# Kernel tuning notes

Measured on AMD Instinct MI355X. Metric: run time of the kernel, lower is better.

## Reference

```python
import jax, jax.numpy as jnp
import numpy as np
import math

_PI = math.pi

@jax.custom_vjp
def atan_spike(h):
    # Heaviside forward, ATan surrogate (alpha=2.0) backward
    return (h >= 0).astype(h.dtype)

def _atan_fwd(h):
    return (h >= 0).astype(h.dtype), h

def _atan_bwd(h, g):
    # d/dh [ (1/pi) atan(pi*h) + 1/2 ] = 1 / (1 + (pi*h)^2)
    return (g / (1.0 + (_PI * h) ** 2),)

atan_spike.defvjp(_atan_fwd, _atan_bwd)

def plif_scan(x, alpha, v_th):
    # x: [T, ...]; PLIF: v += alpha*(x - v); spike; hard reset to 0
    a = alpha.reshape(())
    def step(v, xt):
        v = v + a * (xt - v)
        s = atan_spike(v - v_th)
        v = v * (1.0 - s)
        return v, s
    v0 = jnp.zeros_like(x[0])
    _, spikes = jax.lax.scan(step, v0, x)
    return spikes

def setup_inputs() -> dict:
    key = jax.random.key(0)
    k1, k2, k3 = jax.random.split(key, 3)
    T, B, N, D, H = 4, 8, 1024, 512, 2048
    x = jax.random.normal(k1, (T, B, N, D), dtype=jnp.float32)
    W1 = jax.random.normal(k2, (H, D), dtype=jnp.float32) * (1.0 / math.sqrt(D))
    W2 = jax.random.normal(k3, (D, H), dtype=jnp.float32) * (1.0 / math.sqrt(H))
    alpha1 = jnp.full((1,), 0.5, dtype=jnp.float32)  # 1/tau, tau=2.0
    alpha2 = jnp.full((1,), 0.5, dtype=jnp.float32)
    return {"x": x, "W1": W1, "W2": W2, "alpha1": alpha1, "alpha2": alpha2}

def reference(x, W1, W2, alpha1, alpha2):
    V_TH = 1.0
    h = jnp.einsum('tbnd,hd->tbnh', x, W1)      # fc1 (no bias)
    s1 = plif_scan(h, alpha1, V_TH)             # PLIF neuron 1
    y = jnp.einsum('tbnh,dh->tbnd', s1, W2)     # fc2 (no bias)
    s2 = plif_scan(y, alpha2, V_TH)             # PLIF neuron 2
    return s2
```

## Files before the change

### kernel.cpp

```cpp
#include <hip/hip_runtime.h>

#define T_  4
#define BN_ 8192
#define D_  512
#define H_  2048

typedef float f4 __attribute__((ext_vector_type(4)));
typedef float f32x4 __attribute__((ext_vector_type(4)));
typedef _Float16 f16x8 __attribute__((ext_vector_type(8)));

__device__ __forceinline__ void split8(const f4 u0, const f4 u1, f16x8& hi, f16x8& lo) {
#pragma unroll
    for (int i = 0; i < 4; ++i) {
        _Float16 a = (_Float16)u0[i]; hi[i]     = a; lo[i]     = (_Float16)(u0[i] - (float)a);
        _Float16 b = (_Float16)u1[i]; hi[4 + i] = b; lo[4 + i] = (_Float16)(u1[i] - (float)b);
    }
}

__device__ __forceinline__ void spikes4_to_f16(unsigned b, unsigned& lo, unsigned& hi) {
    const unsigned p0 = (b & 0xFFu) | ((b & 0xFF00u) << 8);
    const unsigned p1 = ((b >> 16) & 0xFFu) | ((b >> 8) & 0xFF0000u);
    lo = p0 * 0x3C00u;
    hi = p1 * 0x3C00u;
}

__device__ __forceinline__ void glds16(const void* g, void* l) {
    __builtin_amdgcn_global_load_lds((const __attribute__((address_space(1))) unsigned int*)g,
                                     (__attribute__((address_space(3))) unsigned int*)l, 16, 0, 0);
}

__global__ __launch_bounds__(256)
void k_split(const float* __restrict__ x, _Float16* __restrict__ xs)
{
    const int b   = blockIdx.x;
    const int t   = b & 3;
    const int k0B = (b >> 2) & 15;
    const int bnB = b >> 6;
    const int kg  = threadIdx.x & 3;
    const int row = threadIdx.x >> 2;

    const float* src = x + ((size_t)t * BN_ + bnB * 64 + row) * D_ + k0B * 32 + kg * 8;
    const f4 u0 = *(const f4*)src;
    const f4 u1 = *(const f4*)(src + 4);
    f16x8 hi, lo;
    split8(u0, u1, hi, lo);

    const size_t base = ((size_t)(bnB * 16 + k0B) * 4 + t) * 4096;
    *(f16x8*)&xs[base +        kg * 512 + row * 8] = hi;
    *(f16x8*)&xs[base + 2048 + kg * 512 + row * 8] = lo;
}

__global__ __launch_bounds__(256)
void k_splitW(const float* __restrict__ W1, _Float16* __restrict__ w1s)
{
    const int gid = blockIdx.x * 256 + threadIdx.x;
    const int col = gid & 127;
    const int kg  = (gid >> 7) & 3;
    const int kb  = (gid >> 9) & 15;
    const int h0b = gid >> 13;

    const float* src = W1 + (size_t)(h0b * 128 + col) * D_ + kb * 32 + kg * 8;
    const f4 u0 = *(const f4*)src;
    const f4 u1 = *(const f4*)(src + 4);
    f16x8 hi, lo;
    split8(u0, u1, hi, lo);

    const size_t base = (size_t)(h0b * 16 + kb) * 8192;
    *(f16x8*)&w1s[base +        kg * 1024 + col * 8] = hi;
    *(f16x8*)&w1s[base + 4096 + kg * 1024 + col * 8] = lo;
}

__global__ __launch_bounds__(256, 2)
void k_fc1b(const _Float16* __restrict__ xs, const _Float16* __restrict__ w1s,
            const float* __restrict__ alphap, unsigned char* __restrict__ s1)
{
    __shared__ _Float16 Ab[2][T_][2][4][64][8];

    const int tid  = threadIdx.x;
    const int lane = tid & 63;
    const int w    = tid >> 6;
    const int wr   = (w >> 1) * 32;
    const int wc   = (w & 1) * 64;

    const int gid   = blockIdx.x;
    const int panel = gid >> 8;
    const int h0i   = (gid >> 4) & 15;
    const int bnL   = gid & 15;
    const int bnB   = panel * 16 + bnL;
    const int bn0   = bnB * 64;
    const int h0    = h0i * 128;

    const int l15 = lane & 15;
    const int kgl = lane >> 4;
    const int lq  = kgl * 4;

    const float a1v = alphap[0];

    f32x4 acc[T_][2][4];
#pragma unroll
    for (int t = 0; t < T_; ++t)
#pragma unroll
        for (int m = 0; m < 2; ++m)
#pragma unroll
            for (int n = 0; n < 4; ++n) acc[t][m][n] = (f32x4){0.f, 0.f, 0.f, 0.f};

    const char* xbase = (const char*)xs + (size_t)bnB * 16 * 32768;
    const _Float16* bl = w1s + (size_t)h0i * (16 * 8192)
                             + (size_t)kgl * 1024 + (size_t)(wc + l15) * 8;

#define FC1_GLDS(BUF, KB)                                                        \
    {                                                                            \
        const char* cb_ = xbase + (size_t)(KB) * 32768;                          \
        _Float16* lA_ = &Ab[BUF][0][0][0][0][0];                                 \
        _Pragma("unroll")                                                        \
        for (int i_ = 0; i_ < 8; ++i_) {                                         \
            const int c_ = i_ * 4 + w;                                           \
            glds16(cb_ + c_ * 1024 + lane * 16, lA_ + c_ * 512);                 \
        }                                                                        \
    }

#define FC1_BLOAD(KB, B0, B1)                                                    \
    {                                                                            \
        const _Float16* bp_ = bl + (size_t)(KB) * 8192;                          \
        _Pragma("unroll")                                                        \
        for (int n_ = 0; n_ < 4; ++n_) {                                         \
            B0[n_] = *(const f16x8*)(bp_ + n_ * 128);                            \
            B1[n_] = *(const f16x8*)(bp_ + 4096 + n_ * 128);                     \
        }                                                                        \
    }

#define FC1_COMPUTE(BUF, B0, B1)                                                 \
    _Pragma("unroll")                                                            \
    for (int t_ = 0; t_ < T_; ++t_)                                              \
        _Pragma("unroll")                                                        \
        for (int m_ = 0; m_ < 2; ++m_) {                                         \
            const f16x8 a0_ = *(const f16x8*)&Ab[BUF][t_][0][kgl][wr + m_ * 16 + l15][0]; \
            const f16x8 a1_ = *(const f16x8*)&Ab[BUF][t_][1][kgl][wr + m_ * 16 + l15][0]; \
            _Pragma("unroll")                                                    \
            for (int n_ = 0; n_ < 4; ++n_) {                                     \
                acc[t_][m_][n_] = __builtin_amdgcn_mfma_f32_16x16x32_f16(a0_, B0[n_], acc[t_][m_][n_], 0, 0, 0); \
                acc[t_][m_][n_] = __builtin_amdgcn_mfma_f32_16x16x32_f16(a0_, B1[n_], acc[t_][m_][n_], 0, 0, 0); \
                acc[t_][m_][n_] = __builtin_amdgcn_mfma_f32_16x16x32_f16(a1_, B0[n_], acc[t_][m_][n_], 0, 0, 0); \
            }                                                                    \
        }

    f16x8 bA0[4], bA1[4], bB0[4], bB1[4];

    FC1_GLDS(0, 0)
    FC1_BLOAD(0, bA0, bA1)
    __syncthreads();

#pragma unroll 1
    for (int it = 0; it < 8; ++it) {
        const int kb = 2 * it;
        FC1_GLDS(1, kb + 1)
        FC1_BLOAD(kb + 1, bB0, bB1)
        FC1_COMPUTE(0, bA0, bA1)
        __syncthreads();
        if (it < 7) {
            FC1_GLDS(0, kb + 2)
            FC1_BLOAD(kb + 2, bA0, bA1)
        }
        FC1_COMPUTE(1, bB0, bB1)
        __syncthreads();
    }

#pragma unroll
    for (int m = 0; m < 2; ++m)
#pragma unroll
        for (int n = 0; n < 4; ++n)
#pragma unroll
            for (int q = 0; q < 4; ++q) {
                float v = 0.f;
#pragma unroll
                for (int t = 0; t < T_; ++t) {
                    v = v + a1v * (acc[t][m][n][q] - v);
                    const bool sp = (v >= 1.0f);
                    s1[((size_t)t * BN_ + bn0 + wr + m * 16 + lq + q) * H_ +
                       (h0 + wc + n * 16 + l15)] = sp ? (unsigned char)1 : (unsigned char)0;
                    if (sp) v = 0.f;
                }
            }
}

__global__ __launch_bounds__(256, 2)
void k_fc1(const _Float16* __restrict__ xs, const float* __restrict__ W1,
           const float* __restrict__ alphap, unsigned char* __restrict__ s1)
{
    __shared__ _Float16 Ab[T_][2][4][64][8];
    __shared__ _Float16 Bb[2][4][128][8];

    const int tid  = threadIdx.x;
    const int lane = tid & 63;
    const int w    = tid >> 6;
    const int wr   = (w >> 1) * 32;
    const int wc   = (w & 1) * 64;
    const int bnB  = blockIdx.x;
    const int bn0  = bnB * 64;
    const int h0   = blockIdx.y * 128;

    const int l15 = lane & 15;
    const int kgl = lane >> 4;
    const int lq  = kgl * 4;

    const int bcol = tid & 127;
    const int bkh  = tid >> 7;

    const float a1v = alphap[0];

    f32x4 acc[T_][2][4];
#pragma unroll
    for (int t = 0; t < T_; ++t)
#pragma unroll
        for (int m = 0; m < 2; ++m)
#pragma unroll
            for (int n = 0; n < 4; ++n) acc[t][m][n] = (f32x4){0.f, 0.f, 0.f, 0.f};

    const char* xbase = (const char*)xs + (size_t)bnB * 16 * 32768;
    const float* wp0  = W1 + (size_t)(h0 + bcol) * D_ + bkh * 16;

    f4 w0 = *(const f4*)wp0,       w1 = *(const f4*)(wp0 + 4);
    f4 w2 = *(const f4*)(wp0 + 8), w3 = *(const f4*)(wp0 + 12);

    for (int kb = 0; kb < 16; ++kb) {
        __syncthreads();
        const char* cb = xbase + (size_t)kb * 32768;
        _Float16* lA = &Ab[0][0][0][0][0];
#pragma unroll
        for (int i = 0; i < 8; ++i) {
            const int c = i * 4 + w;
            glds16(cb + c * 1024 + lane * 16, lA + c * 512);
        }
        {
            f16x8 hA, lA2, hB, lB;
            split8(w0, w1, hA, lA2); split8(w2, w3, hB, lB);
            *(f16x8*)&Bb[0][2 * bkh][bcol][0]     = hA;
            *(f16x8*)&Bb[0][2 * bkh + 1][bcol][0] = hB;
            *(f16x8*)&Bb[1][2 * bkh][bcol][0]     = lA2;
            *(f16x8*)&Bb[1][2 * bkh + 1][bcol][0] = lB;
        }
        if (kb < 15) {
            const float* wp = wp0 + (kb + 1) * 32;
            w0 = *(const f4*)wp;       w1 = *(const f4*)(wp + 4);
            w2 = *(const f4*)(wp + 8); w3 = *(const f4*)(wp + 12);
        }
        __syncthreads();

        f16x8 bf0[4], bf1[4];
#pragma unroll
        for (int n = 0; n < 4; ++n) {
            bf0[n] = *(const f16x8*)&Bb[0][kgl][wc + n * 16 + l15][0];
            bf1[n] = *(const f16x8*)&Bb[1][kgl][wc + n * 16 + l15][0];
        }
#pragma unroll
        for (int t = 0; t < T_; ++t)
#pragma unroll
            for (int m = 0; m < 2; ++m) {
                const f16x8 a0 = *(const f16x8*)&Ab[t][0][kgl][wr + m * 16 + l15][0];
                const f16x8 a1 = *(const f16x8*)&Ab[t][1][kgl][wr + m * 16 + l15][0];
#pragma unroll
                for (int n = 0; n < 4; ++n) {
                    acc[t][m][n] = __builtin_amdgcn_mfma_f32_16x16x32_f16(a0, bf0[n], acc[t][m][n], 0, 0, 0);
                    acc[t][m][n] = __builtin_amdgcn_mfma_f32_16x16x32_f16(a0, bf1[n], acc[t][m][n], 0, 0, 0);
                    acc[t][m][n] = __builtin_amdgcn_mfma_f32_16x16x32_f16(a1, bf0[n], acc[t][m][n], 0, 0, 0);
                }
            }
    }

#pragma unroll
    for (int m = 0; m < 2; ++m)
#pragma unroll
        for (int n = 0; n < 4; ++n)
#pragma unroll
            for (int q = 0; q < 4; ++q) {
                float v = 0.f;
#pragma unroll
                for (int t = 0; t < T_; ++t) {
                    v = v + a1v * (acc[t][m][n][q] - v);
                    const bool sp = (v >= 1.0f);
                    s1[((size_t)t * BN_ + bn0 + wr + m * 16 + lq + q) * H_ +
                       (h0 + wc + n * 16 + l15)] = sp ? (unsigned char)1 : (unsigned char)0;
                    if (sp) v = 0.f;
                }
            }
}

__global__ __launch_bounds__(256, 2)
void k_fc2(const unsigned char* __restrict__ s1, const float* __restrict__ W2,
           const float* __restrict__ alphap, float* __restrict__ out)
{
    __shared__ _Float16 A2[2][4][4][64][8];
    __shared__ _Float16 B2[2][2][4][128][8];

    const int tid  = threadIdx.x;
    const int lane = tid & 63;
    const int w    = tid >> 6;
    const int wr   = (w >> 1) * 32;
    const int wc   = (w & 1) * 64;
    const int bn0  = blockIdx.x * 64;
    const int d0   = blockIdx.y * 128;

    const int l15 = lane & 15;
    const int kgl = lane >> 4;
    const int lq  = kgl * 4;

    const int bcol = tid & 127;
    const int bkh  = tid >> 7;
    const int at   = tid >> 6;
    const int arow = lane;

    const float a2v = alphap[0];

    f32x4 acc[T_][2][4];
#pragma unroll
    for (int t = 0; t < T_; ++t)
#pragma unroll
        for (int m = 0; m < 2; ++m)
#pragma unroll
            for (int n = 0; n < 4; ++n) acc[t][m][n] = (f32x4){0.f, 0.f, 0.f, 0.f};

    const unsigned char* ap = s1 + ((size_t)at * BN_ + bn0 + arow) * H_;
    const float*         wp0 = W2 + (size_t)(d0 + bcol) * H_ + bkh * 16;

    {
        const uint4 r0 = *(const uint4*)(ap);
        const uint4 r1 = *(const uint4*)(ap + 16);
        unsigned v[8];
        spikes4_to_f16(r0.x, v[0], v[1]); spikes4_to_f16(r0.y, v[2], v[3]);
        spikes4_to_f16(r0.z, v[4], v[5]); spikes4_to_f16(r0.w, v[6], v[7]);
        *(uint4*)&A2[0][at][0][arow][0] = *(const uint4*)&v[0];
        *(uint4*)&A2[0][at][1][arow][0] = *(const uint4*)&v[4];
        spikes4_to_f16(r1.x, v[0], v[1]); spikes4_to_f16(r1.y, v[2], v[3]);
        spikes4_to_f16(r1.z, v[4], v[5]); spikes4_to_f16(r1.w, v[6], v[7]);
        *(uint4*)&A2[0][at][2][arow][0] = *(const uint4*)&v[0];
        *(uint4*)&A2[0][at][3][arow][0] = *(const uint4*)&v[4];

        const f4 w0 = *(const f4*)wp0, w1 = *(const f4*)(wp0 + 4);
        const f4 w2 = *(const f4*)(wp0 + 8), w3 = *(const f4*)(wp0 + 12);
        f16x8 hA, lA, hB, lB;
        split8(w0, w1, hA, lA); split8(w2, w3, hB, lB);
        *(f16x8*)&B2[0][0][2 * bkh][bcol][0]     = hA;
        *(f16x8*)&B2[0][0][2 * bkh + 1][bcol][0] = hB;
        *(f16x8*)&B2[0][1][2 * bkh][bcol][0]     = lA;
        *(f16x8*)&B2[0][1][2 * bkh + 1][bcol][0] = lB;
    }
    __syncthreads();

    int cur = 0;
    for (int kb = 0; kb < 64; ++kb) {
        uint4 r0, r1; f4 w0, w1, w2, w3;
        if (kb < 63) {
            r0 = *(const uint4*)(ap + (kb + 1) * 32);
            r1 = *(const uint4*)(ap + (kb + 1) * 32 + 16);
            const float* wp = wp0 + (kb + 1) * 32;
            w0 = *(const f4*)wp;       w1 = *(const f4*)(wp + 4);
            w2 = *(const f4*)(wp + 8); w3 = *(const f4*)(wp + 12);
        }

        f16x8 bf0[4], bf1[4];
#pragma unroll
        for (int n = 0; n < 4; ++n) {
            bf0[n] = *(const f16x8*)&B2[cur][0][kgl][wc + n * 16 + l15][0];
            bf1[n] = *(const f16x8*)&B2[cur][1][kgl][wc + n * 16 + l15][0];
        }
#pragma unroll
        for (int t = 0; t < T_; ++t)
#pragma unroll
            for (int m = 0; m < 2; ++m) {
                const f16x8 af = *(const f16x8*)&A2[cur][t][kgl][wr + m * 16 + l15][0];
#pragma unroll
                for (int n = 0; n < 4; ++n) {
                    acc[t][m][n] = __builtin_amdgcn_mfma_f32_16x16x32_f16(af, bf0[n], acc[t][m][n], 0, 0, 0);
                    acc[t][m][n] = __builtin_amdgcn_mfma_f32_16x16x32_f16(af, bf1[n], acc[t][m][n], 0, 0, 0);
                }
            }

        if (kb < 63) {
            unsigned v[8];
            spikes4_to_f16(r0.x, v[0], v[1]); spikes4_to_f16(r0.y, v[2], v[3]);
            spikes4_to_f16(r0.z, v[4], v[5]); spikes4_to_f16(r0.w, v[6], v[7]);
            *(uint4*)&A2[cur ^ 1][at][0][arow][0] = *(const uint4*)&v[0];
            *(uint4*)&A2[cur ^ 1][at][1][arow][0] = *(const uint4*)&v[4];
            spikes4_to_f16(r1.x, v[0], v[1]); spikes4_to_f16(r1.y, v[2], v[3]);
            spikes4_to_f16(r1.z, v[4], v[5]); spikes4_to_f16(r1.w, v[6], v[7]);
            *(uint4*)&A2[cur ^ 1][at][2][arow][0] = *(const uint4*)&v[0];
            *(uint4*)&A2[cur ^ 1][at][3][arow][0] = *(const uint4*)&v[4];

            f16x8 hA, lA, hB, lB;
            split8(w0, w1, hA, lA); split8(w2, w3, hB, lB);
            *(f16x8*)&B2[cur ^ 1][0][2 * bkh][bcol][0]     = hA;
            *(f16x8*)&B2[cur ^ 1][0][2 * bkh + 1][bcol][0] = hB;
            *(f16x8*)&B2[cur ^ 1][1][2 * bkh][bcol][0]     = lA;
            *(f16x8*)&B2[cur ^ 1][1][2 * bkh + 1][bcol][0] = lB;
        }
        __syncthreads();
        cur ^= 1;
    }

#pragma unroll
    for (int m = 0; m < 2; ++m)
#pragma unroll
        for (int n = 0; n < 4; ++n)
#pragma unroll
            for (int q = 0; q < 4; ++q) {
                float v = 0.f;
#pragma unroll
                for (int t = 0; t < T_; ++t) {
                    v = v + a2v * (acc[t][m][n][q] - v);
                    const bool sp = (v >= 1.0f);
                    out[((size_t)t * BN_ + bn0 + wr + m * 16 + lq + q) * D_ +
                        (d0 + wc + n * 16 + l15)] = sp ? 1.0f : 0.0f;
                    if (sp) v = 0.f;
                }
            }
}

extern "C" void kernel_launch(void* const* d_in, const int* in_sizes, int n_in,
                              void* d_out, int out_size, void* d_ws, size_t ws_size,
                              hipStream_t stream) {
    const float* x      = (const float*)d_in[0];
    const float* W1     = (const float*)d_in[1];
    const float* W2     = (const float*)d_in[2];
    const float* alpha1 = (const float*)d_in[3];
    const float* alpha2 = (const float*)d_in[4];
    float* out = (float*)d_out;

    unsigned char* s1 = (unsigned char*)d_ws;
    _Float16* xs = (_Float16*)d_out;
    const size_t S1_BYTES = (size_t)T_ * BN_ * H_;
    const size_t W1S_BYTES = (size_t)H_ * D_ * 2 * sizeof(_Float16);

    k_split<<<dim3(8192), dim3(256), 0, stream>>>(x, xs);

    if (ws_size >= S1_BYTES + W1S_BYTES) {
        _Float16* w1s = (_Float16*)((char*)d_ws + S1_BYTES);
        k_splitW<<<dim3(512), dim3(256), 0, stream>>>(W1, w1s);
        k_fc1b<<<dim3(2048), dim3(256), 0, stream>>>(xs, w1s, alpha1, s1);
    } else {
        k_fc1<<<dim3(128, 16), dim3(256), 0, stream>>>(xs, W1, alpha1, s1);
    }
    k_fc2<<<dim3(128, 4), dim3(256), 0, stream>>>(s1, W2, alpha2, out);
}
```

Measured before the change: 310.0 us.

## Pre-split W2 into fp16 hi/lo tiles and stream B operands from registers in fc2

Adds a k_splitW2 kernel that converts W2 once into MFMA-ready fp16 hi/lo tiles in the workspace. A new k_fc2b loads these B fragments straight into registers with prefetch, so only the spike A tile is staged in LDS with double buffering. The fc1b main loop changes from a manually two-way unrolled loop to a single loop with a buffer index and register copies. This trades an extra prep kernel and more workspace for less LDS traffic and no per-block fp32-to-fp16 splitting of W2.

```diff
diff --git a/kernel.cpp b/kernel.cpp
--- a/kernel.cpp
+++ b/kernel.cpp
@@ -68,6 +68,26 @@
     const size_t base = (size_t)(h0b * 16 + kb) * 8192;
     *(f16x8*)&w1s[base +        kg * 1024 + col * 8] = hi;
     *(f16x8*)&w1s[base + 4096 + kg * 1024 + col * 8] = lo;
+}
+
+__global__ __launch_bounds__(256)
+void k_splitW2(const float* __restrict__ W2, _Float16* __restrict__ w2s)
+{
+    const int gid = blockIdx.x * 256 + threadIdx.x;
+    const int col = gid & 127;
+    const int kg  = (gid >> 7) & 3;
+    const int kb  = (gid >> 9) & 63;
+    const int d0b = gid >> 15;
+
+    const float* src = W2 + (size_t)(d0b * 128 + col) * H_ + kb * 32 + kg * 8;
+    const f4 u0 = *(const f4*)src;
+    const f4 u1 = *(const f4*)(src + 4);
+    f16x8 hi, lo;
+    split8(u0, u1, hi, lo);
+
+    const size_t base = (size_t)(d0b * 64 + kb) * 8192;
+    *(f16x8*)&w2s[base +        kg * 1024 + col * 8] = hi;
+    *(f16x8*)&w2s[base + 4096 + kg * 1024 + col * 8] = lo;
 }
 
 __global__ __launch_bounds__(256, 2)
@@ -144,25 +164,25 @@
             }                                                                    \
         }
 
-    f16x8 bA0[4], bA1[4], bB0[4], bB1[4];
+    f16x8 bc0[4], bc1[4], bpA0[4], bpA1[4];
 
     FC1_GLDS(0, 0)
-    FC1_BLOAD(0, bA0, bA1)
+    FC1_BLOAD(0, bc0, bc1)
     __syncthreads();
 
-#pragma unroll 1
-    for (int it = 0; it < 8; ++it) {
-        const int kb = 2 * it;
-        FC1_GLDS(1, kb + 1)
-        FC1_BLOAD(kb + 1, bB0, bB1)
-        FC1_COMPUTE(0, bA0, bA1)
+    int buf = 0;
+    for (int kb = 0; kb < 16; ++kb) {
+        if (kb < 15) {
+            FC1_GLDS(buf ^ 1, kb + 1)
+            FC1_BLOAD(kb + 1, bpA0, bpA1)
+        }
+        FC1_COMPUTE(buf, bc0, bc1)
         __syncthreads();
-        if (it < 7) {
-            FC1_GLDS(0, kb + 2)
-            FC1_BLOAD(kb + 2, bA0, bA1)
-        }
-        FC1_COMPUTE(1, bB0, bB1)
-        __syncthreads();
+        if (kb < 15) {
+#pragma unroll
+            for (int n = 0; n < 4; ++n) { bc0[n] = bpA0[n]; bc1[n] = bpA1[n]; }
+        }
+        buf ^= 1;
     }
 
 #pragma unroll
@@ -280,6 +300,125 @@
                     const bool sp = (v >= 1.0f);
                     s1[((size_t)t * BN_ + bn0 + wr + m * 16 + lq + q) * H_ +
                        (h0 + wc + n * 16 + l15)] = sp ? (unsigned char)1 : (unsigned char)0;
+                    if (sp) v = 0.f;
+                }
+            }
+}
+
+__global__ __launch_bounds__(256, 2)
+void k_fc2b(const unsigned char* __restrict__ s1, const _Float16* __restrict__ w2s,
+            const float* __restrict__ alphap, float* __restrict__ out)
+{
+    __shared__ _Float16 A2[2][T_][4][64][8];
+
+    const int tid  = threadIdx.x;
+    const int lane = tid & 63;
+    const int w    = tid >> 6;
+    const int wr   = (w >> 1) * 32;
+    const int wc   = (w & 1) * 64;
+    const int bn0  = blockIdx.x * 64;
+    const int d0i  = blockIdx.y;
+    const int d0   = d0i * 128;
+
+    const int l15 = lane & 15;
+    const int kgl = lane >> 4;
+    const int lq  = kgl * 4;
+
+    const int at   = w;
+    const int arow = lane;
+
+    const float a2v = alphap[0];
+
+    f32x4 acc[T_][2][4];
+#pragma unroll
+    for (int t = 0; t < T_; ++t)
+#pragma unroll
+        for (int m = 0; m < 2; ++m)
+#pragma unroll
+            for (int n = 0; n < 4; ++n) acc[t][m][n] = (f32x4){0.f, 0.f, 0.f, 0.f};
+
+    const unsigned char* ap = s1 + ((size_t)at * BN_ + bn0 + arow) * H_;
+    const _Float16* bl = w2s + (size_t)d0i * (64 * 8192)
+                             + (size_t)kgl * 1024 + (size_t)(wc + l15) * 8;
+
+#define FC2_ACONV_WRITE(BUF, R0, R1)                                             \
+    {                                                                            \
+        unsigned v_[8];                                                          \
+        spikes4_to_f16(R0.x, v_[0], v_[1]); spikes4_to_f16(R0.y, v_[2], v_[3]);  \
+        spikes4_to_f16(R0.z, v_[4], v_[5]); spikes4_to_f16(R0.w, v_[6], v_[7]);  \
+        *(uint4*)&A2[BUF][at][0][arow][0] = *(const uint4*)&v_[0];               \
+        *(uint4*)&A2[BUF][at][1][arow][0] = *(const uint4*)&v_[4];               \
+        spikes4_to_f16(R1.x, v_[0], v_[1]); spikes4_to_f16(R1.y, v_[2], v_[3]);  \
+        spikes4_to_f16(R1.z, v_[4], v_[5]); spikes4_to_f16(R1.w, v_[6], v_[7]);  \
+        *(uint4*)&A2[BUF][at][2][arow][0] = *(const uint4*)&v_[0];               \
+        *(uint4*)&A2[BUF][at][3][arow][0] = *(const uint4*)&v_[4];               \
+    }
+
+#define FC2_BLOAD(KB, B0, B1)                                                    \
+    {                                                                            \
+        const _Float16* bp_ = bl + (size_t)(KB) * 8192;                          \
+        _Pragma("unroll")                                                        \
+        for (int n_ = 0; n_ < 4; ++n_) {                                         \
+            B0[n_] = *(const f16x8*)(bp_ + n_ * 128);                            \
+            B1[n_] = *(const f16x8*)(bp_ + 4096 + n_ * 128);                     \
+        }                                                                        \
+    }
+
+    f16x8 bc0[4], bc1[4], bpA0[4], bpA1[4];
+
+    {
+        const uint4 r0 = *(const uint4*)(ap);
+        const uint4 r1 = *(const uint4*)(ap + 16);
+        FC2_ACONV_WRITE(0, r0, r1)
+        FC2_BLOAD(0, bc0, bc1)
+    }
+    __syncthreads();
+
+    int cur = 0;
+    for (int kb = 0; kb < 64; ++kb) {
+        uint4 r0, r1;
+        if (kb < 63) {
+            r0 = *(const uint4*)(ap + (kb + 1) * 32);
+            r1 = *(const uint4*)(ap + (kb + 1) * 32 + 16);
+            FC2_BLOAD(kb + 1, bpA0, bpA1)
+        }
+
+#pragma unroll
+        for (int t = 0; t < T_; ++t)
+#pragma unroll
+            for (int m = 0; m < 2; ++m) {
+                const f16x8 af = *(const f16x8*)&A2[cur][t][kgl][wr + m * 16 + l15][0];
+#pragma unroll
+                for (int n = 0; n < 4; ++n) {
+                    acc[t][m][n] = __builtin_amdgcn_mfma_f32_16x16x32_f16(af, bc0[n], acc[t][m][n], 0, 0, 0);
+                    acc[t][m][n] = __builtin_amdgcn_mfma_f32_16x16x32_f16(af, bc1[n], acc[t][m][n], 0, 0, 0);
+                }
+            }
+
+        if (kb < 63) {
+            FC2_ACONV_WRITE(cur ^ 1, r0, r1)
+        }
+        __syncthreads();
+        if (kb < 63) {
+#pragma unroll
+            for (int n = 0; n < 4; ++n) { bc0[n] = bpA0[n]; bc1[n] = bpA1[n]; }
+        }
+        cur ^= 1;
+    }
+
+#pragma unroll
+    for (int m = 0; m < 2; ++m)
+#pragma unroll
+        for (int n = 0; n < 4; ++n)
+#pragma unroll
+            for (int q = 0; q < 4; ++q) {
+                float v = 0.f;
+#pragma unroll
+                for (int t = 0; t < T_; ++t) {
+                    v = v + a2v * (acc[t][m][n][q] - v);
+                    const bool sp = (v >= 1.0f);
+                    out[((size_t)t * BN_ + bn0 + wr + m * 16 + lq + q) * D_ +
+                        (d0 + wc + n * 16 + l15)] = sp ? 1.0f : 0.0f;
                     if (sp) v = 0.f;
                 }
             }
@@ -427,17 +566,28 @@
 
     unsigned char* s1 = (unsigned char*)d_ws;
     _Float16* xs = (_Float16*)d_out;
-    const size_t S1_BYTES = (size_t)T_ * BN_ * H_;
+    const size_t S1_BYTES  = (size_t)T_ * BN_ * H_;
     const size_t W1S_BYTES = (size_t)H_ * D_ * 2 * sizeof(_Float16);
+    const size_t W2S_BYTES = (size_t)D_ * H_ * 2 * sizeof(_Float16);
 
     k_split<<<dim3(8192), dim3(256), 0, stream>>>(x, xs);
 
-    if (ws_size >= S1_BYTES + W1S_BYTES) {
+    const bool haveW1 = ws_size >= S1_BYTES + W1S_BYTES;
+    const bool haveW2 = ws_size >= S1_BYTES + W1S_BYTES + W2S_BYTES;
+
+    if (haveW1) {
         _Float16* w1s = (_Float16*)((char*)d_ws + S1_BYTES);
         k_splitW<<<dim3(512), dim3(256), 0, stream>>>(W1, w1s);
         k_fc1b<<<dim3(2048), dim3(256), 0, stream>>>(xs, w1s, alpha1, s1);
     } else {
         k_fc1<<<dim3(128, 16), dim3(256), 0, stream>>>(xs, W1, alpha1, s1);
     }
-    k_fc2<<<dim3(128, 4), dim3(256), 0, stream>>>(s1, W2, alpha2, out);
-}
+
+    if (haveW2) {
+        _Float16* w2s = (_Float16*)((char*)d_ws + S1_BYTES + W1S_BYTES);
+        k_splitW2<<<dim3(512), dim3(256), 0, stream>>>(W2, w2s);
+        k_fc2b<<<dim3(128, 4), dim3(256), 0, stream>>>(s1, w2s, alpha2, out);
+    } else {
+        k_fc2<<<dim3(128, 4), dim3(256), 0, stream>>>(s1, W2, alpha2, out);
+    }
+}
```

Result: faster. 295.8 us (-4.6%).
